# Kernel tuning notes

Hardware: AMD Instinct MI355X
Metric: run time of the kernel (lower is better)

## Reference

```python
import jax, jax.numpy as jnp
import numpy as np

D_IN = 2048
D_OUT = 2048
NUM_HEADS = 16
HEAD_DIM = D_OUT // NUM_HEADS


def setup_inputs() -> dict:
    key = jax.random.key(0)
    ks = jax.random.split(key, 6)
    b, t = 2, 2048
    x = jax.random.normal(ks[0], (b, t, D_IN), dtype=jnp.float32)
    s = 0.02
    Wq = jax.random.normal(ks[1], (D_OUT, D_IN), dtype=jnp.float32) * s
    Wk = jax.random.normal(ks[2], (D_OUT, D_IN), dtype=jnp.float32) * s
    Wv = jax.random.normal(ks[3], (D_OUT, D_IN), dtype=jnp.float32) * s
    Wo = jax.random.normal(ks[4], (D_OUT, D_OUT), dtype=jnp.float32) * s
    bo = jnp.zeros((D_OUT,), dtype=jnp.float32)
    theta = (10000.0 ** (-jnp.arange(0, HEAD_DIM, 2, dtype=jnp.float32) / HEAD_DIM))
    return {"x": x, "Wq": Wq, "Wk": Wk, "Wv": Wv, "Wo": Wo, "bo": bo, "theta": theta}


def _rope(v, sin, cos):
    # v: [b, t, h, d]; split even/odd feature indices, rotate, concat halves
    ve, vo = v[..., ::2], v[..., 1::2]
    return jnp.concatenate([ve * cos - vo * sin, ve * sin + vo * cos], axis=-1)


def reference(x, Wq, Wk, Wv, Wo, bo, theta):
    b, t, _ = x.shape
    q = (x @ Wq.T).reshape(b, t, NUM_HEADS, HEAD_DIM)
    k = (x @ Wk.T).reshape(b, t, NUM_HEADS, HEAD_DIM)
    v = (x @ Wv.T).reshape(b, t, NUM_HEADS, HEAD_DIM)

    pos = jnp.arange(t, dtype=jnp.float32)[:, None]          # [t, 1]
    freq = pos * theta[None, :]                              # [t, d/2]
    sin = jnp.sin(freq)[None, :, None, :]                    # [1, t, 1, d/2]
    cos = jnp.cos(freq)[None, :, None, :]
    q = _rope(q, sin, cos)
    k = _rope(k, sin, cos)

    # [b, h, t, t]
    scores = jnp.einsum('bqhd,bkhd->bhqk', q, k)
    causal = jnp.triu(jnp.ones((t, t), dtype=bool), k=1)
    scores = jnp.where(causal[None, None], -jnp.inf, scores)
    attn = jax.nn.softmax(scores / jnp.sqrt(jnp.float32(HEAD_DIM)), axis=-1)

    ctx = jnp.einsum('bhqk,bkhd->bqhd', attn, v).reshape(b, t, D_OUT)
    return ctx @ Wo.T + bo
```

## Files before the change

kernel.cpp:

```cpp
#include <hip/hip_runtime.h>

typedef unsigned short ushortT;
typedef short short8 __attribute__((ext_vector_type(8)));
typedef float floatx4 __attribute__((ext_vector_type(4)));

#define D_MODEL 2048
#define HEAD_DIM 128
#define NUM_HEADS 16
#define SEQ 2048
#define BATCH 2
#define M_TOK (BATCH * SEQ)
#define QKV_ELEMS ((size_t)M_TOK * D_MODEL)
#define W_ELEMS ((size_t)D_MODEL * D_MODEL)

__device__ __forceinline__ float bf2f(ushortT h) {
    return __uint_as_float(((unsigned int)h) << 16);
}
__device__ __forceinline__ ushortT f2bf(float f) {
    unsigned int u = __float_as_uint(f);
    u = u + 0x7fffu + ((u >> 16) & 1u);
    return (ushortT)(u >> 16);
}

__device__ __forceinline__ void gload_lds16(const ushortT* g, short* lds_wave_base) {
    __builtin_amdgcn_global_load_lds(
        (const __attribute__((address_space(1))) unsigned int*)g,
        (__attribute__((address_space(3))) unsigned int*)lds_wave_base,
        16, 0, 0);
}

__global__ __launch_bounds__(256) void cvt_all(
    const float* __restrict__ x,  const float* __restrict__ wq,
    const float* __restrict__ wk, const float* __restrict__ wv,
    const float* __restrict__ wo,
    ushortT* __restrict__ xb,  ushortT* __restrict__ wqb,
    ushortT* __restrict__ wkb, ushortT* __restrict__ wvb,
    ushortT* __restrict__ wob)
{
    const size_t XC = QKV_ELEMS / 8;
    const size_t WC = W_ELEMS / 8;
    size_t c = (size_t)blockIdx.x * 256 + threadIdx.x;
    const float* s; ushortT* d;
    if (c < XC)              { s = x;  d = xb;  }
    else if ((c -= XC) < WC) { s = wq; d = wqb; }
    else if ((c -= WC) < WC) { s = wk; d = wkb; }
    else if ((c -= WC) < WC) { s = wv; d = wvb; }
    else     { c -= WC;        s = wo; d = wob; }
    const float* f = s + c * 8;
    floatx4 a = *(const floatx4*)f;
    floatx4 b = *(const floatx4*)(f + 4);
    short8 r;
    r[0] = (short)f2bf(a.x); r[1] = (short)f2bf(a.y);
    r[2] = (short)f2bf(a.z); r[3] = (short)f2bf(a.w);
    r[4] = (short)f2bf(b.x); r[5] = (short)f2bf(b.y);
    r[6] = (short)f2bf(b.z); r[7] = (short)f2bf(b.w);
    *(short8*)(d + c * 8) = r;
}

template<bool OUTF32>
__global__ __launch_bounds__(256) void gemm_bt(
    const ushortT* __restrict__ A,
    const ushortT* __restrict__ W0, const ushortT* __restrict__ W1,
    const ushortT* __restrict__ W2,
    void* C0, void* C1, void* C2, const float* __restrict__ bias)
{
    __shared__ short As[128 * 32];
    __shared__ short Bs[128 * 32];

    const int z = blockIdx.z;
    const ushortT* W = (z == 0) ? W0 : (z == 1 ? W1 : W2);
    void* C = (z == 0) ? C0 : (z == 1 ? C1 : C2);

    const int tid  = threadIdx.x;
    const int wave = tid >> 6;
    const int lane = tid & 63;
    const int lr   = lane & 15;
    const int quad = lane >> 4;
    const int wm   = (wave & 1) * 64;
    const int wn   = (wave >> 1) * 64;

    const int blockM = blockIdx.y * 128;
    const int blockN = blockIdx.x * 128;

    const int srow = tid >> 2;
    const int scol = (tid & 3) * 8;
    const ushortT* ag = A + (size_t)(blockM + srow) * D_MODEL + scol;
    const ushortT* wg = W + (size_t)(blockN + srow) * D_MODEL + scol;
    short* al = As + wave * 512;
    short* bl = Bs + wave * 512;

    floatx4 acc[4][4];
    #pragma unroll
    for (int i = 0; i < 4; i++)
        #pragma unroll
        for (int j = 0; j < 4; j++) acc[i][j] = (floatx4){0.f, 0.f, 0.f, 0.f};

    for (int kk = 0; kk < D_MODEL; kk += 32) {
        gload_lds16(ag + kk,                 al);
        gload_lds16(ag + kk + 64 * D_MODEL,  al + 64 * 32);
        gload_lds16(wg + kk,                 bl);
        gload_lds16(wg + kk + 64 * D_MODEL,  bl + 64 * 32);
        __syncthreads();

        short8 af[4], bf[4];
        #pragma unroll
        for (int s = 0; s < 4; s++) {
            af[s] = *(const short8*)&As[(wm + s * 16 + lr) * 32 + quad * 8];
            bf[s] = *(const short8*)&Bs[(wn + s * 16 + lr) * 32 + quad * 8];
        }
        #pragma unroll
        for (int sm = 0; sm < 4; sm++)
            #pragma unroll
            for (int sn = 0; sn < 4; sn++)
                acc[sm][sn] = __builtin_amdgcn_mfma_f32_16x16x32_bf16(
                    af[sm], bf[sn], acc[sm][sn], 0, 0, 0);
        __syncthreads();
    }

    #pragma unroll
    for (int sm = 0; sm < 4; sm++) {
        const int row = blockM + wm + sm * 16 + quad * 4;
        #pragma unroll
        for (int sn = 0; sn < 4; sn++) {
            const int col = blockN + wn + sn * 16 + lr;
            const float bval = bias ? bias[col] : 0.f;
            #pragma unroll
            for (int rr = 0; rr < 4; rr++) {
                const float val = acc[sm][sn][rr] + bval;
                if constexpr (OUTF32)
                    ((float*)C)[(size_t)(row + rr) * D_MODEL + col] = val;
                else
                    ((ushortT*)C)[(size_t)(row + rr) * D_MODEL + col] = f2bf(val);
            }
        }
    }
}

__global__ __launch_bounds__(256) void rope_kernel(
    ushortT* __restrict__ qb, ushortT* __restrict__ kb,
    const float* __restrict__ theta)
{
    const int tok = blockIdx.x;
    ushortT* p = (blockIdx.y ? kb : qb) + (size_t)tok * D_MODEL;
    const int t = tok & (SEQ - 1);
    const int tid = threadIdx.x;
    const int d = tid & 63;
    const int hb = tid >> 6;

    const float fr = (float)t * theta[d];
    const float s = sinf(fr);
    const float c = cosf(fr);

    float ve[4], vo[4];
    #pragma unroll
    for (int i = 0; i < 4; i++) {
        ushortT* ph = p + (i * 4 + hb) * HEAD_DIM;
        ve[i] = bf2f(ph[2 * d]);
        vo[i] = bf2f(ph[2 * d + 1]);
    }
    __syncthreads();
    #pragma unroll
    for (int i = 0; i < 4; i++) {
        ushortT* ph = p + (i * 4 + hb) * HEAD_DIM;
        ph[d]      = f2bf(ve[i] * c - vo[i] * s);
        ph[d + 64] = f2bf(ve[i] * s + vo[i] * c);
    }
}

__global__ __launch_bounds__(256) void kpack_kernel(
    const ushortT* __restrict__ k, ushortT* __restrict__ kf)
{
    const int kt16 = blockIdx.x;
    const int bh   = blockIdx.y;
    const int b = bh >> 4, h = bh & 15;
    const int tid = threadIdx.x;
    const int ks = tid >> 6, lane = tid & 63;
    const int lr = lane & 15, quad = lane >> 4;
    short8 v = *(const short8*)(
        k + (size_t)(b * SEQ + kt16 * 16 + lr) * D_MODEL + h * HEAD_DIM + ks * 32 + quad * 8);
    *(short8*)(kf + ((size_t)(bh * 128 + kt16) * 4 + ks) * 512 + lane * 8) = v;
}

__global__ __launch_bounds__(256) void vpack_kernel(
    const ushortT* __restrict__ v, ushortT* __restrict__ vf)
{
    __shared__ ushortT tile[32][136];
    const int ct = blockIdx.x;
    const int bh = blockIdx.y;
    const int b = bh >> 4, h = bh & 15;
    const int tid = threadIdx.x;

    const int tt = tid >> 3;
    const int dc = (tid & 7) * 16;
    const ushortT* src = v + (size_t)(b * SEQ + ct * 32 + tt) * D_MODEL + h * HEAD_DIM + dc;
    *(short8*)&tile[tt][dc]     = *(const short8*)src;
    *(short8*)&tile[tt][dc + 8] = *(const short8*)(src + 8);
    __syncthreads();

    const int w = tid >> 6, lane = tid & 63;
    const int lr = lane & 15, quad = lane >> 4;
    #pragma unroll
    for (int p = 0; p < 2; p++) {
        const int rt = w + p * 4;
        short8 out;
        #pragma unroll
        for (int j = 0; j < 8; j++)
            out[j] = (short)tile[quad * 8 + j][rt * 16 + lr];
        *(short8*)(vf + ((size_t)(bh * 8 + rt) * 64 + ct) * 512 + lane * 8) = out;
    }
}

__global__ __launch_bounds__(256) void flash_attn2(
    const ushortT* __restrict__ q, const ushortT* __restrict__ kf,
    const ushortT* __restrict__ vf, ushortT* __restrict__ ctx)
{
    __shared__ short Kt[16 * 512];
    __shared__ short Vt[16 * 512];
    __shared__ short Pl[4][16][72];

    const unsigned lid = blockIdx.x;
    const int xcd  = lid & 7;
    const int slot = lid >> 3;
    const int ih   = slot >> 4;
    const int qtb  = slot & 15;
    const int bh   = (ih << 3) | xcd;

    const int b = bh >> 4, h = bh & 15;
    const size_t base = (size_t)b * SEQ * D_MODEL + h * HEAD_DIM;
    const size_t kfb = (size_t)bh * 128 * 4 * 512;
    const size_t vfb = (size_t)bh * 8 * 64 * 512;
    const int tid = threadIdx.x;
    const int w = tid >> 6, lane = tid & 63;
    const int lr = lane & 15, quad = lane >> 4;
    short* myP = &Pl[w][0][0];

    for (int pass = 0; pass < 2; pass++) {
        const int qt = (pass == 0) ? qtb : (SEQ / 64 - 1 - qtb);
        const int q0 = qt * 64 + w * 16;

        short8 Qf[4];
        {
            const ushortT* qrow = q + base + (size_t)(q0 + lr) * D_MODEL + quad * 8;
            #pragma unroll
            for (int ks = 0; ks < 4; ks++) {
                short8 raw = *(const short8*)(qrow + ks * 32);
                #pragma unroll
                for (int j = 0; j < 8; j++)
                    Qf[ks][j] = (short)f2bf(bf2f((ushortT)raw[j]) * 0.08838834764831845f);
            }
        }

        floatx4 Of[8];
        #pragma unroll
        for (int i = 0; i < 8; i++) Of[i] = (floatx4){0.f, 0.f, 0.f, 0.f};
        float m_i[4] = {-INFINITY, -INFINITY, -INFINITY, -INFINITY};
        float l_i[4] = {0.f, 0.f, 0.f, 0.f};

        for (int kt0 = 0; kt0 <= qt * 64; kt0 += 64) {
            {
                const ushortT* ksrc = kf + kfb + (size_t)kt0 * 128;
                #pragma unroll
                for (int c = 0; c < 4; c++)
                    gload_lds16(ksrc + c * 2048 + tid * 8, Kt + c * 2048 + w * 512);
                #pragma unroll
                for (int c = 0; c < 4; c++) {
                    const int e   = c * 2048 + tid * 8;
                    const int dsub = e >> 10;
                    const int rem  = e & 1023;
                    const ushortT* vsrc = vf + vfb +
                        ((size_t)dsub * 64 + (kt0 >> 5) + (rem >> 9)) * 512 + (rem & 511);
                    gload_lds16(vsrc, Vt + c * 2048 + w * 512);
                }
            }
            __syncthreads();

            floatx4 Sf[4];
            #pragma unroll
            for (int sub = 0; sub < 4; sub++) {
                floatx4 acc = {0.f, 0.f, 0.f, 0.f};
                #pragma unroll
                for (int ks = 0; ks < 4; ks++) {
                    short8 Kf_ = *(const short8*)(Kt + (sub * 4 + ks) * 512 + lane * 8);
                    acc = __builtin_amdgcn_mfma_f32_16x16x32_bf16(Qf[ks], Kf_, acc, 0, 0, 0);
                }
                Sf[sub] = acc;
            }

            short8 Vr[16];
            #pragma unroll
            for (int dsub = 0; dsub < 8; dsub++) {
                Vr[2 * dsub]     = *(const short8*)(Vt + dsub * 1024 + lane * 8);
                Vr[2 * dsub + 1] = *(const short8*)(Vt + dsub * 1024 + 512 + lane * 8);
            }

            if (kt0 == qt * 64) {
                #pragma unroll
                for (int sub = 0; sub < 4; sub++) {
                    const int ktg = kt0 + sub * 16 + lr;
                    #pragma unroll
                    for (int i = 0; i < 4; i++)
                        if (ktg > q0 + quad * 4 + i) Sf[sub][i] = -1e30f;
                }
            }

            float mn[4], alpha[4], rs[4];
            #pragma unroll
            for (int i = 0; i < 4; i++) {
                float t = fmaxf(fmaxf(Sf[0][i], Sf[1][i]), fmaxf(Sf[2][i], Sf[3][i]));
                t = fmaxf(t, __shfl_xor(t, 1));
                t = fmaxf(t, __shfl_xor(t, 2));
                t = fmaxf(t, __shfl_xor(t, 4));
                t = fmaxf(t, __shfl_xor(t, 8));
                mn[i] = fmaxf(m_i[i], t);
                alpha[i] = __expf(m_i[i] - mn[i]);
                m_i[i] = mn[i];
                rs[i] = 0.f;
            }
            #pragma unroll
            for (int sub = 0; sub < 4; sub++) {
                #pragma unroll
                for (int i = 0; i < 4; i++) {
                    const float p = __expf(Sf[sub][i] - mn[i]);
                    rs[i] += p;
                    myP[(quad * 4 + i) * 72 + sub * 16 + lr] = (short)f2bf(p);
                }
            }
            #pragma unroll
            for (int i = 0; i < 4; i++) {
                float t = rs[i];
                t += __shfl_xor(t, 1);
                t += __shfl_xor(t, 2);
                t += __shfl_xor(t, 4);
                t += __shfl_xor(t, 8);
                l_i[i] = l_i[i] * alpha[i] + t;
            }
            #pragma unroll
            for (int dsub = 0; dsub < 8; dsub++)
                #pragma unroll
                for (int i = 0; i < 4; i++) Of[dsub][i] *= alpha[i];

            asm volatile("s_waitcnt lgkmcnt(0)" ::: "memory");
            short8 Pf0 = *(const short8*)(myP + lr * 72 + quad * 8);
            short8 Pf1 = *(const short8*)(myP + lr * 72 + 32 + quad * 8);

            #pragma unroll
            for (int dsub = 0; dsub < 8; dsub++) {
                Of[dsub] = __builtin_amdgcn_mfma_f32_16x16x32_bf16(
                    Pf0, Vr[2 * dsub], Of[dsub], 0, 0, 0);
                Of[dsub] = __builtin_amdgcn_mfma_f32_16x16x32_bf16(
                    Pf1, Vr[2 * dsub + 1], Of[dsub], 0, 0, 0);
            }
            __syncthreads();
        }

        float inv[4];
        #pragma unroll
        for (int i = 0; i < 4; i++) inv[i] = 1.f / l_i[i];
        #pragma unroll
        for (int dsub = 0; dsub < 8; dsub++)
            #pragma unroll
            for (int i = 0; i < 4; i++)
                ctx[base + (size_t)(q0 + quad * 4 + i) * D_MODEL + dsub * 16 + lr] =
                    f2bf(Of[dsub][i] * inv[i]);
    }
}

extern "C" void kernel_launch(void* const* d_in, const int* in_sizes, int n_in,
                              void* d_out, int out_size, void* d_ws, size_t ws_size,
                              hipStream_t stream) {
    const float* x     = (const float*)d_in[0];
    const float* Wq    = (const float*)d_in[1];
    const float* Wk    = (const float*)d_in[2];
    const float* Wv    = (const float*)d_in[3];
    const float* Wo    = (const float*)d_in[4];
    const float* bo    = (const float*)d_in[5];
    const float* theta = (const float*)d_in[6];

    ushortT* ws  = (ushortT*)d_ws;
    ushortT* qb  = ws;
    ushortT* kb  = ws + QKV_ELEMS;
    ushortT* vb  = ws + 2 * QKV_ELEMS;
    ushortT* kfb = ws + 3 * QKV_ELEMS;
    ushortT* xb  = kfb;
    ushortT* wqb = ws + 4 * QKV_ELEMS;
    ushortT* wkb = wqb + W_ELEMS;
    ushortT* wvb = wkb + W_ELEMS;
    ushortT* wob = wvb + W_ELEMS;

    cvt_all<<<dim3((unsigned)((QKV_ELEMS / 8 + 4 * (W_ELEMS / 8)) / 256)), 256, 0, stream>>>(
        x, Wq, Wk, Wv, Wo, xb, wqb, wkb, wvb, wob);

    gemm_bt<false><<<dim3(D_MODEL / 128, M_TOK / 128, 3), 256, 0, stream>>>(
        xb, wqb, wkb, wvb, qb, kb, vb, nullptr);

    rope_kernel<<<dim3(M_TOK, 2), 256, 0, stream>>>(qb, kb, theta);

    kpack_kernel<<<dim3(SEQ / 16, BATCH * NUM_HEADS), 256, 0, stream>>>(kb, kfb);

    vpack_kernel<<<dim3(SEQ / 32, BATCH * NUM_HEADS), 256, 0, stream>>>(vb, kb);

    flash_attn2<<<dim3(512), 256, 0, stream>>>(qb, kfb, kb, vb);

    gemm_bt<true><<<dim3(D_MODEL / 128, M_TOK / 128, 1), 256, 0, stream>>>(
        vb, wob, wob, wob, d_out, d_out, d_out, bo);
}
```

Measured before the change: 431.4 us.

## Triple-buffer GEMM with 256x128 tiles, swizzled LDS and async prefetch

Rewrites the projection GEMM to use 512-thread blocks computing 256x128 tiles with BK=64, a three-slot LDS ring that prefetches two k-steps ahead, and XOR-swizzled LDS columns to avoid bank conflicts. Barriers are replaced with explicit vmcnt waits and s_barrier, and MFMA sections get raised priority. The aim is to hide global-load latency, cut per-iteration syncs and increase operand reuse. LDS use per block grows to 144 KB, which limits occupancy, and the hand-written waitcnt logic risks races.

```diff
diff --git a/kernel.cpp b/kernel.cpp
--- a/kernel.cpp
+++ b/kernel.cpp
@@ -58,14 +58,14 @@
 }
 
 template<bool OUTF32>
-__global__ __launch_bounds__(256) void gemm_bt(
+__global__ __launch_bounds__(512, 2) void gemm_bt(
     const ushortT* __restrict__ A,
     const ushortT* __restrict__ W0, const ushortT* __restrict__ W1,
     const ushortT* __restrict__ W2,
     void* C0, void* C1, void* C2, const float* __restrict__ bias)
 {
-    __shared__ short As[128 * 32];
-    __shared__ short Bs[128 * 32];
+    __shared__ short As[3][256 * 64];
+    __shared__ short Bs[3][128 * 64];
 
     const int z = blockIdx.z;
     const ushortT* W = (z == 0) ? W0 : (z == 1 ? W1 : W2);
@@ -76,18 +76,19 @@
     const int lane = tid & 63;
     const int lr   = lane & 15;
     const int quad = lane >> 4;
-    const int wm   = (wave & 1) * 64;
-    const int wn   = (wave >> 1) * 64;
-
-    const int blockM = blockIdx.y * 128;
+    const int wm   = (wave & 3) * 64;
+    const int wn   = (wave >> 2) * 64;
+
+    const int blockM = blockIdx.y * 256;
     const int blockN = blockIdx.x * 128;
 
-    const int srow = tid >> 2;
-    const int scol = (tid & 3) * 8;
-    const ushortT* ag = A + (size_t)(blockM + srow) * D_MODEL + scol;
-    const ushortT* wg = W + (size_t)(blockN + srow) * D_MODEL + scol;
-    short* al = As + wave * 512;
-    short* bl = Bs + wave * 512;
+    const int srow = tid >> 3;
+    const int scol = (tid & 7) * 8;
+    const int scolSwz = scol ^ ((srow & 7) << 3);
+    const ushortT* Ag = A + (size_t)(blockM + srow) * D_MODEL + scolSwz;
+    const ushortT* Wg = W + (size_t)(blockN + srow) * D_MODEL + scolSwz;
+
+    const int rswz = (lr & 7) << 3;
 
     floatx4 acc[4][4];
     #pragma unroll
@@ -95,38 +96,81 @@
         #pragma unroll
         for (int j = 0; j < 4; j++) acc[i][j] = (floatx4){0.f, 0.f, 0.f, 0.f};
 
-    for (int kk = 0; kk < D_MODEL; kk += 32) {
-        gload_lds16(ag + kk,                 al);
-        gload_lds16(ag + kk + 64 * D_MODEL,  al + 64 * 32);
-        gload_lds16(wg + kk,                 bl);
-        gload_lds16(wg + kk + 64 * D_MODEL,  bl + 64 * 32);
-        __syncthreads();
-
-        short8 af[4], bf[4];
-        #pragma unroll
-        for (int s = 0; s < 4; s++) {
-            af[s] = *(const short8*)&As[(wm + s * 16 + lr) * 32 + quad * 8];
-            bf[s] = *(const short8*)&Bs[(wn + s * 16 + lr) * 32 + quad * 8];
+    constexpr int NT = D_MODEL / 64;
+
+    #pragma unroll
+    for (int i = 0; i < 4; i++)
+        gload_lds16(Ag + (size_t)i * 64 * D_MODEL, &As[0][i * 4096 + wave * 512]);
+    #pragma unroll
+    for (int j = 0; j < 2; j++)
+        gload_lds16(Wg + (size_t)j * 64 * D_MODEL, &Bs[0][j * 4096 + wave * 512]);
+    #pragma unroll
+    for (int i = 0; i < 4; i++)
+        gload_lds16(Ag + 64 + (size_t)i * 64 * D_MODEL, &As[1][i * 4096 + wave * 512]);
+    #pragma unroll
+    for (int j = 0; j < 2; j++)
+        gload_lds16(Wg + 64 + (size_t)j * 64 * D_MODEL, &Bs[1][j * 4096 + wave * 512]);
+    asm volatile("s_waitcnt vmcnt(6)" ::: "memory");
+    __builtin_amdgcn_s_barrier();
+    asm volatile("" ::: "memory");
+
+    int slot = 0;
+    for (int t = 0; t < NT; ++t) {
+        if (t + 2 < NT) {
+            const int s2 = (slot + 2 >= 3) ? slot - 1 : slot + 2;
+            const size_t kk = (size_t)(t + 2) * 64;
+            #pragma unroll
+            for (int i = 0; i < 4; i++)
+                gload_lds16(Ag + kk + (size_t)i * 64 * D_MODEL,
+                            &As[s2][i * 4096 + wave * 512]);
+            #pragma unroll
+            for (int j = 0; j < 2; j++)
+                gload_lds16(Wg + kk + (size_t)j * 64 * D_MODEL,
+                            &Bs[s2][j * 4096 + wave * 512]);
         }
         #pragma unroll
-        for (int sm = 0; sm < 4; sm++)
-            #pragma unroll
-            for (int sn = 0; sn < 4; sn++)
-                acc[sm][sn] = __builtin_amdgcn_mfma_f32_16x16x32_bf16(
-                    af[sm], bf[sn], acc[sm][sn], 0, 0, 0);
-        __syncthreads();
-    }
-
-    #pragma unroll
-    for (int sm = 0; sm < 4; sm++) {
-        const int row = blockM + wm + sm * 16 + quad * 4;
-        #pragma unroll
-        for (int sn = 0; sn < 4; sn++) {
-            const int col = blockN + wn + sn * 16 + lr;
+        for (int p = 0; p < 2; p++) {
+            const int cbase = (p * 32 + quad * 8) ^ rswz;
+            short8 af[4], bf[4];
+            #pragma unroll
+            for (int fr = 0; fr < 4; fr++)
+                af[fr] = *(const short8*)&As[slot][(wm + fr * 16 + lr) * 64 + cbase];
+            #pragma unroll
+            for (int fc = 0; fc < 4; fc++)
+                bf[fc] = *(const short8*)&Bs[slot][(wn + fc * 16 + lr) * 64 + cbase];
+            __builtin_amdgcn_s_setprio(1);
+            #pragma unroll
+            for (int fr = 0; fr < 4; fr++)
+                #pragma unroll
+                for (int fc = 0; fc < 4; fc++)
+                    acc[fr][fc] = __builtin_amdgcn_mfma_f32_16x16x32_bf16(
+                        af[fr], bf[fc], acc[fr][fc], 0, 0, 0);
+            __builtin_amdgcn_s_setprio(0);
+            if (p == 0) {
+                __builtin_amdgcn_s_barrier();
+                asm volatile("" ::: "memory");
+            } else {
+                if (t < NT - 2)
+                    asm volatile("s_waitcnt vmcnt(6)" ::: "memory");
+                else
+                    asm volatile("s_waitcnt vmcnt(0)" ::: "memory");
+                __builtin_amdgcn_s_barrier();
+                asm volatile("" ::: "memory");
+            }
+        }
+        slot = (slot + 1 >= 3) ? 0 : slot + 1;
+    }
+
+    #pragma unroll
+    for (int fr = 0; fr < 4; fr++) {
+        const int row = blockM + wm + fr * 16 + quad * 4;
+        #pragma unroll
+        for (int fc = 0; fc < 4; fc++) {
+            const int col = blockN + wn + fc * 16 + lr;
             const float bval = bias ? bias[col] : 0.f;
             #pragma unroll
             for (int rr = 0; rr < 4; rr++) {
-                const float val = acc[sm][sn][rr] + bval;
+                const float val = acc[fr][fc][rr] + bval;
                 if constexpr (OUTF32)
                     ((float*)C)[(size_t)(row + rr) * D_MODEL + col] = val;
                 else
@@ -390,7 +434,7 @@
     cvt_all<<<dim3((unsigned)((QKV_ELEMS / 8 + 4 * (W_ELEMS / 8)) / 256)), 256, 0, stream>>>(
         x, Wq, Wk, Wv, Wo, xb, wqb, wkb, wvb, wob);
 
-    gemm_bt<false><<<dim3(D_MODEL / 128, M_TOK / 128, 3), 256, 0, stream>>>(
+    gemm_bt<false><<<dim3(D_MODEL / 128, M_TOK / 256, 3), 512, 0, stream>>>(
         xb, wqb, wkb, wvb, qb, kb, vb, nullptr);
 
     rope_kernel<<<dim3(M_TOK, 2), 256, 0, stream>>>(qb, kb, theta);
@@ -401,6 +445,6 @@
 
     flash_attn2<<<dim3(512), 256, 0, stream>>>(qb, kfb, kb, vb);
 
-    gemm_bt<true><<<dim3(D_MODEL / 128, M_TOK / 128, 1), 256, 0, stream>>>(
+    gemm_bt<true><<<dim3(D_MODEL / 128, M_TOK / 256, 1), 512, 0, stream>>>(
         vb, wob, wob, wob, d_out, d_out, d_out, bo);
 }
```

Measured after the change: 457.3 us. 6.0% more time.

## Double-buffer K/V tiles in flash attention to overlap loads with compute

Applied to the files above, without the earlier changes.

Splits the LDS K and V tiles into two buffers and issues the async global-to-LDS load for the next key tile while the current tile's QK and PV MFMAs run. The single per-iteration __syncthreads is replaced by an explicit vmcnt wait plus barrier at the end of each iteration. This aims to hide global memory latency behind compute, at the cost of doubled LDS use for K/V (64KB), which may reduce occupancy.

```diff
diff --git a/kernel.cpp b/kernel.cpp
--- a/kernel.cpp
+++ b/kernel.cpp
@@ -214,8 +214,8 @@
     const ushortT* __restrict__ q, const ushortT* __restrict__ kf,
     const ushortT* __restrict__ vf, ushortT* __restrict__ ctx)
 {
-    __shared__ short Kt[16 * 512];
-    __shared__ short Vt[16 * 512];
+    __shared__ short Kt[2][16 * 512];
+    __shared__ short Vt[2][16 * 512];
     __shared__ short Pl[4][16][72];
 
     const unsigned lid = blockIdx.x;
@@ -234,6 +234,22 @@
     const int lr = lane & 15, quad = lane >> 4;
     short* myP = &Pl[w][0][0];
 
+    auto stage_tile = [&](int kt0, int buf) {
+        const ushortT* ksrc = kf + kfb + (size_t)kt0 * 128;
+        #pragma unroll
+        for (int c = 0; c < 4; c++)
+            gload_lds16(ksrc + c * 2048 + tid * 8, &Kt[buf][c * 2048 + w * 512]);
+        #pragma unroll
+        for (int c = 0; c < 4; c++) {
+            const int e    = c * 2048 + tid * 8;
+            const int dsub = e >> 10;
+            const int rem  = e & 1023;
+            const ushortT* vsrc = vf + vfb +
+                ((size_t)dsub * 64 + (kt0 >> 5) + (rem >> 9)) * 512 + (rem & 511);
+            gload_lds16(vsrc, &Vt[buf][c * 2048 + w * 512]);
+        }
+    };
+
     for (int pass = 0; pass < 2; pass++) {
         const int qt = (pass == 0) ? qtb : (SEQ / 64 - 1 - qtb);
         const int q0 = qt * 64 + w * 16;
@@ -256,23 +272,15 @@
         float m_i[4] = {-INFINITY, -INFINITY, -INFINITY, -INFINITY};
         float l_i[4] = {0.f, 0.f, 0.f, 0.f};
 
-        for (int kt0 = 0; kt0 <= qt * 64; kt0 += 64) {
-            {
-                const ushortT* ksrc = kf + kfb + (size_t)kt0 * 128;
-                #pragma unroll
-                for (int c = 0; c < 4; c++)
-                    gload_lds16(ksrc + c * 2048 + tid * 8, Kt + c * 2048 + w * 512);
-                #pragma unroll
-                for (int c = 0; c < 4; c++) {
-                    const int e   = c * 2048 + tid * 8;
-                    const int dsub = e >> 10;
-                    const int rem  = e & 1023;
-                    const ushortT* vsrc = vf + vfb +
-                        ((size_t)dsub * 64 + (kt0 >> 5) + (rem >> 9)) * 512 + (rem & 511);
-                    gload_lds16(vsrc, Vt + c * 2048 + w * 512);
-                }
-            }
-            __syncthreads();
+        stage_tile(0, 0);
+        asm volatile("s_waitcnt vmcnt(0)" ::: "memory");
+        __builtin_amdgcn_s_barrier();
+        asm volatile("" ::: "memory");
+
+        const int ntiles = qt + 1;
+        for (int t = 0; t < ntiles; ++t) {
+            const int buf = t & 1;
+            const int kt0 = t * 64;
 
             floatx4 Sf[4];
             #pragma unroll
@@ -280,7 +288,7 @@
                 floatx4 acc = {0.f, 0.f, 0.f, 0.f};
                 #pragma unroll
                 for (int ks = 0; ks < 4; ks++) {
-                    short8 Kf_ = *(const short8*)(Kt + (sub * 4 + ks) * 512 + lane * 8);
+                    short8 Kf_ = *(const short8*)(&Kt[buf][(sub * 4 + ks) * 512 + lane * 8]);
                     acc = __builtin_amdgcn_mfma_f32_16x16x32_bf16(Qf[ks], Kf_, acc, 0, 0, 0);
                 }
                 Sf[sub] = acc;
@@ -289,9 +297,11 @@
             short8 Vr[16];
             #pragma unroll
             for (int dsub = 0; dsub < 8; dsub++) {
-                Vr[2 * dsub]     = *(const short8*)(Vt + dsub * 1024 + lane * 8);
-                Vr[2 * dsub + 1] = *(const short8*)(Vt + dsub * 1024 + 512 + lane * 8);
-            }
+                Vr[2 * dsub]     = *(const short8*)(&Vt[buf][dsub * 1024 + lane * 8]);
+                Vr[2 * dsub + 1] = *(const short8*)(&Vt[buf][dsub * 1024 + 512 + lane * 8]);
+            }
+
+            if (t + 1 < ntiles) stage_tile((t + 1) * 64, buf ^ 1);
 
             if (kt0 == qt * 64) {
                 #pragma unroll
@@ -306,12 +316,12 @@
             float mn[4], alpha[4], rs[4];
             #pragma unroll
             for (int i = 0; i < 4; i++) {
-                float t = fmaxf(fmaxf(Sf[0][i], Sf[1][i]), fmaxf(Sf[2][i], Sf[3][i]));
-                t = fmaxf(t, __shfl_xor(t, 1));
-                t = fmaxf(t, __shfl_xor(t, 2));
-                t = fmaxf(t, __shfl_xor(t, 4));
-                t = fmaxf(t, __shfl_xor(t, 8));
-                mn[i] = fmaxf(m_i[i], t);
+                float t2 = fmaxf(fmaxf(Sf[0][i], Sf[1][i]), fmaxf(Sf[2][i], Sf[3][i]));
+                t2 = fmaxf(t2, __shfl_xor(t2, 1));
+                t2 = fmaxf(t2, __shfl_xor(t2, 2));
+                t2 = fmaxf(t2, __shfl_xor(t2, 4));
+                t2 = fmaxf(t2, __shfl_xor(t2, 8));
+                mn[i] = fmaxf(m_i[i], t2);
                 alpha[i] = __expf(m_i[i] - mn[i]);
                 m_i[i] = mn[i];
                 rs[i] = 0.f;
@@ -327,12 +337,12 @@
             }
             #pragma unroll
             for (int i = 0; i < 4; i++) {
-                float t = rs[i];
-                t += __shfl_xor(t, 1);
-                t += __shfl_xor(t, 2);
-                t += __shfl_xor(t, 4);
-                t += __shfl_xor(t, 8);
-                l_i[i] = l_i[i] * alpha[i] + t;
+                float t2 = rs[i];
+                t2 += __shfl_xor(t2, 1);
+                t2 += __shfl_xor(t2, 2);
+                t2 += __shfl_xor(t2, 4);
+                t2 += __shfl_xor(t2, 8);
+                l_i[i] = l_i[i] * alpha[i] + t2;
             }
             #pragma unroll
             for (int dsub = 0; dsub < 8; dsub++)
@@ -350,7 +360,10 @@
                 Of[dsub] = __builtin_amdgcn_mfma_f32_16x16x32_bf16(
                     Pf1, Vr[2 * dsub + 1], Of[dsub], 0, 0, 0);
             }
-            __syncthreads();
+
+            asm volatile("s_waitcnt vmcnt(0)" ::: "memory");
+            __builtin_amdgcn_s_barrier();
+            asm volatile("" ::: "memory");
         }
 
         float inv[4];
```

New measurement: 432.9 us. No clear change (+0.3%).
